# Performance work log

Measured on AMD Instinct MI355X. Metric: run time of the kernel, lower is better.

The kernel has to match this reference:

```python
import jax, jax.numpy as jnp
import numpy as np

INPUT_DIM = 512
EMBED_DIM = 64
B, S = 4, 4096


def setup_inputs() -> dict:
    key = jax.random.key(0)
    ks = jax.random.split(key, 9)
    scale = 1.0 / np.sqrt(INPUT_DIM)
    return {
        "q": jax.random.normal(ks[0], (B, S, INPUT_DIM), dtype=jnp.float32),
        "k": jax.random.normal(ks[1], (B, S, INPUT_DIM), dtype=jnp.float32),
        "v": jax.random.normal(ks[2], (B, S, INPUT_DIM), dtype=jnp.float32),
        "Wq": jax.random.uniform(ks[3], (INPUT_DIM, EMBED_DIM), jnp.float32, -scale, scale),
        "bq": jax.random.uniform(ks[4], (EMBED_DIM,), jnp.float32, -scale, scale),
        "Wk": jax.random.uniform(ks[5], (INPUT_DIM, EMBED_DIM), jnp.float32, -scale, scale),
        "bk": jax.random.uniform(ks[6], (EMBED_DIM,), jnp.float32, -scale, scale),
        "Wv": jax.random.uniform(ks[7], (INPUT_DIM, EMBED_DIM), jnp.float32, -scale, scale),
        "bv": jax.random.uniform(ks[8], (EMBED_DIM,), jnp.float32, -scale, scale),
    }


def reference(q, k, v, Wq, bq, Wk, bk, Wv, bv):
    # Linear projections (torch Linear: x @ W^T + b; here W stored as [in, out])
    Q = q @ Wq + bq  # [B, S, E]
    K = k @ Wk + bk  # [B, S, E]
    V = v @ Wv + bv  # [B, S, E]
    d_k = K.shape[-1]
    scores = jnp.einsum("bqe,bke->bqk", Q, K) / jnp.sqrt(jnp.float32(d_k))  # [B, S, S]
    attn = jax.nn.softmax(scores, axis=-1)
    return jnp.einsum("bqk,bke->bqe", attn, V)  # [B, S, E]
```

## Files before the change

### kernel.cpp

```cpp
#include <hip/hip_runtime.h>
#include <math.h>

#define S_ 4096
#define C_SCALE 0.18033688011112042f
#define KSPLIT 8

typedef __attribute__((ext_vector_type(4))) float  floatx4;
typedef __attribute__((ext_vector_type(4))) short  short4_t;
typedef __attribute__((ext_vector_type(8))) short  short8_t;
typedef __attribute__((ext_vector_type(4))) unsigned int uintx4;

__device__ __forceinline__ short f2bf(float f) {
  unsigned u = __builtin_bit_cast(unsigned, f);
  u += 0x7FFFu + ((u >> 16) & 1u);
  return (short)(u >> 16);
}
__device__ __forceinline__ unsigned pack2(float lo, float hi) {
  unsigned a = __builtin_bit_cast(unsigned, lo) + 0x8000u;
  unsigned b = __builtin_bit_cast(unsigned, hi) + 0x8000u;
  return __builtin_amdgcn_perm(b, a, 0x07060302u);
}
__device__ __forceinline__ unsigned packt(float lo, float hi) {
  return __builtin_amdgcn_perm(__builtin_bit_cast(unsigned, hi),
                               __builtin_bit_cast(unsigned, lo), 0x07060302u);
}
__device__ __forceinline__ float bf2f(short s) {
  return __builtin_bit_cast(float, (unsigned)((unsigned short)s) << 16);
}
__device__ __forceinline__ void dma16(const void* g, void* l) {
  __builtin_amdgcn_global_load_lds(
      (const __attribute__((address_space(1))) void*)g,
      (__attribute__((address_space(3))) void*)l, 16, 0, 0);
}

__global__ __launch_bounds__(256) void prep_w(const float* __restrict__ Wq,
                                              const float* __restrict__ Wk,
                                              const float* __restrict__ Wv,
                                              short* __restrict__ Wt) {
  __shared__ float T[64 * 65];
  int m = blockIdx.x >> 3, kt = blockIdx.x & 7, tid = threadIdx.x;
  const float* W = (m == 0) ? Wq : (m == 1) ? Wk : Wv;
  float sc = (m == 0) ? C_SCALE : 1.0f;
#pragma unroll
  for (int i = 0; i < 16; i++) {
    int e = i * 256 + tid;
    int k = e >> 6, n = e & 63;
    T[k * 65 + n] = W[(kt * 64 + k) * 64 + n];
  }
  __syncthreads();
#pragma unroll
  for (int i = 0; i < 16; i++) {
    int e = i * 256 + tid;
    int n = e >> 6, k = e & 63;
    Wt[m * 32768 + n * 512 + kt * 64 + k] = f2bf(T[k * 65 + n] * sc);
  }
}

__global__ __launch_bounds__(256, 3) void proj_kernel(
    const float* __restrict__ qin, const float* __restrict__ kin,
    const float* __restrict__ vin, const float* __restrict__ bq,
    const float* __restrict__ bk, const float* __restrict__ bv,
    const short* __restrict__ Wt, short* __restrict__ Qp,
    short* __restrict__ Kp, short* __restrict__ Vt) {
  __shared__ short A_lds[2][64 * 64];

  int tid = threadIdx.x;
  int m = blockIdx.x >> 8;
  int r0 = (blockIdx.x & 255) * 64;
  int wid = tid >> 6, lane = tid & 63, l15 = lane & 15, quad = lane >> 4;

  const float* in = (m == 0) ? qin : (m == 1) ? kin : vin;
  const short* Wm = Wt + m * 32768;

  short8_t wf[8][2];
#pragma unroll
  for (int kc = 0; kc < 8; kc++)
#pragma unroll
    for (int eh = 0; eh < 2; eh++)
      wf[kc][eh] = *(const short8_t*)(Wm + (wid * 16 + l15) * 512 + kc * 64 +
                                      eh * 32 + quad * 8);

  int sr = tid >> 3, sc = tid & 7;
  int sphys = (sc ^ (sr & 7)) * 8;

  floatx4 ar[4];
  auto loadA = [&](int kc) {
    const float* p = in + (size_t)(r0 + sr) * 512 + kc * 64 + sc * 8;
    ar[0] = *(const floatx4*)p;
    ar[1] = *(const floatx4*)(p + 4);
    const float* p2 = p + 32 * 512;
    ar[2] = *(const floatx4*)p2;
    ar[3] = *(const floatx4*)(p2 + 4);
  };

  floatx4 acc[4];
#pragma unroll
  for (int rt = 0; rt < 4; rt++) acc[rt] = (floatx4){0.f, 0.f, 0.f, 0.f};

  loadA(0);
#pragma unroll
  for (int kc = 0; kc < 8; kc++) {
    uintx4 w0 = {pack2(ar[0][0], ar[0][1]), pack2(ar[0][2], ar[0][3]),
                 pack2(ar[1][0], ar[1][1]), pack2(ar[1][2], ar[1][3])};
    uintx4 w1 = {pack2(ar[2][0], ar[2][1]), pack2(ar[2][2], ar[2][3]),
                 pack2(ar[3][0], ar[3][1]), pack2(ar[3][2], ar[3][3])};
    short* Ab = &A_lds[kc & 1][0];
    *(short8_t*)(Ab + sr * 64 + sphys) = __builtin_bit_cast(short8_t, w0);
    *(short8_t*)(Ab + (sr + 32) * 64 + sphys) = __builtin_bit_cast(short8_t, w1);
    __syncthreads();
    if (kc < 7) loadA(kc + 1);
    int akey = l15 & 7;
#pragma unroll
    for (int rt = 0; rt < 4; rt++) {
      int arow = rt * 16 + l15;
#pragma unroll
      for (int eh = 0; eh < 2; eh++) {
        short8_t af = *(const short8_t*)(Ab + arow * 64 + ((eh * 4 + quad) ^ akey) * 8);
        acc[rt] = __builtin_amdgcn_mfma_f32_16x16x32_bf16(af, wf[kc][eh], acc[rt], 0, 0, 0);
      }
    }
  }

  const float* bias = (m == 0) ? bq : (m == 1) ? bk : bv;
  float bsc = (m == 0) ? C_SCALE : 1.0f;
  float bv_ = bias[wid * 16 + l15] * bsc;
  if (m < 2) {
    short* out = (m == 0) ? Qp : Kp;
#pragma unroll
    for (int rt = 0; rt < 4; rt++)
#pragma unroll
      for (int r = 0; r < 4; r++)
        out[(size_t)(r0 + rt * 16 + quad * 4 + r) * 64 + wid * 16 + l15] =
            f2bf(acc[rt][r] + bv_);
  } else {
    int bb = r0 >> 12;
    int s0 = (r0 & 4095);
#pragma unroll
    for (int rt = 0; rt < 4; rt++) {
      short4_t pk = {f2bf(acc[rt][0] + bv_), f2bf(acc[rt][1] + bv_),
                     f2bf(acc[rt][2] + bv_), f2bf(acc[rt][3] + bv_)};
      *(short4_t*)(Vt + (size_t)bb * 262144 + (wid * 16 + l15) * 4096 + s0 +
                   rt * 16 + quad * 4) = pk;
    }
  }
}

__global__ __launch_bounds__(256, 2) void attn_kernel(
    const short* __restrict__ Qp, const short* __restrict__ Kp,
    const short* __restrict__ Vt, short* __restrict__ Po,
    float* __restrict__ Lp) {
  __shared__ short K_lds[2][64 * 64];
  __shared__ short V_lds[2][64 * 64];

  int tid = threadIdx.x;
  int ks = blockIdx.x >> 6, b = (blockIdx.x >> 4) & 3, qt = blockIdx.x & 15;
  int wid = tid >> 6, lane = tid & 63, l15 = lane & 15, quad = lane >> 4;

  const short* Qb = Qp + (size_t)b * (S_ * 64);
  const short* Kb = Kp + (size_t)b * (S_ * 64);
  const short* Vb = Vt + (size_t)b * (64 * S_);

  int q0 = qt * 256 + wid * 64;

  short8_t qf[4][2];
#pragma unroll
  for (int qs = 0; qs < 4; qs++)
#pragma unroll
    for (int h = 0; h < 2; h++)
      qf[qs][h] = *(const short8_t*)(Qb + (q0 + qs * 16 + l15) * 64 + h * 32 + quad * 8);

  floatx4 o[4][4];
#pragma unroll
  for (int qs = 0; qs < 4; qs++)
#pragma unroll
    for (int eb = 0; eb < 4; eb++) o[qs][eb] = (floatx4){0.f, 0.f, 0.f, 0.f};
  float l_acc[4] = {0.f, 0.f, 0.f, 0.f};
  int ks_base = ks * 512;

  auto stage = [&](int t, int buf) {
    int ks0 = ks_base + t * 64;
#pragma unroll
    for (int j = 0; j < 2; j++) {
      int slot = wid * 128 + j * 64 + lane;
      int r = slot >> 3, c = slot & 7;
      int kk = (r & 3) | (((r >> 3) & 1) << 2);
      dma16(Kb + (ks0 + r) * 64 + (c ^ kk) * 8, (void*)&K_lds[buf][(wid * 2 + j) * 512]);
      dma16(Vb + (size_t)r * 4096 + ks0 + (c ^ (r & 7)) * 8,
            (void*)&V_lds[buf][(wid * 2 + j) * 512]);
    }
  };

  stage(0, 0);
  for (int t = 0; t < 8; t++) {
    __syncthreads();
    if (t < 7) stage(t + 1, (t + 1) & 1);
    __syncthreads();
    const short* Kt = K_lds[t & 1];
    const short* Vl = V_lds[t & 1];

    int pr = 8 * (l15 >> 2) + (l15 & 3);
    int kkey = (l15 & 3) | (((l15 >> 2) & 1) << 2);

#pragma unroll
    for (int jg = 0; jg < 2; jg++) {
      const short* Kg = Kt + (jg * 32 + pr) * 64;
      short8_t kA0 = *(const short8_t*)(Kg + ((0 + quad) ^ kkey) * 8);
      short8_t kA1 = *(const short8_t*)(Kg + ((4 + quad) ^ kkey) * 8);
      short8_t kA2 = *(const short8_t*)(Kg + 256 + ((0 + quad) ^ kkey) * 8);
      short8_t kA3 = *(const short8_t*)(Kg + 256 + ((4 + quad) ^ kkey) * 8);
      short8_t vf[4];
#pragma unroll
      for (int eb = 0; eb < 4; eb++)
        vf[eb] = *(const short8_t*)(Vl + (eb * 16 + l15) * 64 +
                                    ((jg * 4 + quad) ^ (l15 & 7)) * 8);
#pragma unroll
      for (int qs = 0; qs < 4; qs++) {
        floatx4 z = (floatx4){0.f, 0.f, 0.f, 0.f};
        floatx4 s0 = __builtin_amdgcn_mfma_f32_16x16x32_bf16(kA0, qf[qs][0], z, 0, 0, 0);
        s0 = __builtin_amdgcn_mfma_f32_16x16x32_bf16(kA1, qf[qs][1], s0, 0, 0, 0);
        floatx4 s1 = __builtin_amdgcn_mfma_f32_16x16x32_bf16(kA2, qf[qs][0], z, 0, 0, 0);
        s1 = __builtin_amdgcn_mfma_f32_16x16x32_bf16(kA3, qf[qs][1], s1, 0, 0, 0);
        float e00 = __builtin_amdgcn_exp2f(s0[0]), e01 = __builtin_amdgcn_exp2f(s0[1]);
        float e02 = __builtin_amdgcn_exp2f(s0[2]), e03 = __builtin_amdgcn_exp2f(s0[3]);
        float e10 = __builtin_amdgcn_exp2f(s1[0]), e11 = __builtin_amdgcn_exp2f(s1[1]);
        float e12 = __builtin_amdgcn_exp2f(s1[2]), e13 = __builtin_amdgcn_exp2f(s1[3]);
        l_acc[qs] += ((e00 + e01) + (e02 + e03)) + ((e10 + e11) + (e12 + e13));
        uintx4 bp = {packt(e00, e01), packt(e02, e03),
                     packt(e10, e11), packt(e12, e13)};
        short8_t pB = __builtin_bit_cast(short8_t, bp);
#pragma unroll
        for (int eb = 0; eb < 4; eb++)
          o[qs][eb] = __builtin_amdgcn_mfma_f32_16x16x32_bf16(vf[eb], pB, o[qs][eb], 0, 0, 0);
      }
    }
  }

#pragma unroll
  for (int qs = 0; qs < 4; qs++) {
    float l = l_acc[qs];
    l += __shfl_xor(l, 16, 64);
    l += __shfl_xor(l, 32, 64);
    int grow = b * 4096 + q0 + qs * 16 + l15;
    short* Pb = Po + ((size_t)ks * 16384 + grow) * 64;
#pragma unroll
    for (int eb = 0; eb < 4; eb++) {
      short4_t pk = {f2bf(o[qs][eb][0]), f2bf(o[qs][eb][1]),
                     f2bf(o[qs][eb][2]), f2bf(o[qs][eb][3])};
      *(short4_t*)(Pb + eb * 16 + quad * 4) = pk;
    }
    if (quad == 0) Lp[ks * 16384 + grow] = l;
  }
}

__global__ __launch_bounds__(256) void combine_kernel(
    const short* __restrict__ Po, const float* __restrict__ Lp,
    float* __restrict__ out) {
  int gid = blockIdx.x * 256 + threadIdx.x;
  int grow = gid >> 3, e0 = (gid & 7) * 8;
  float s[8];
#pragma unroll
  for (int i = 0; i < 8; i++) s[i] = 0.f;
  float l = 0.f;
#pragma unroll
  for (int ks = 0; ks < KSPLIT; ks++) {
    short8_t p = *(const short8_t*)(Po + ((size_t)ks * 16384 + grow) * 64 + e0);
#pragma unroll
    for (int i = 0; i < 8; i++) s[i] += bf2f(p[i]);
    l += Lp[ks * 16384 + grow];
  }
  float inv = 1.0f / l;
  floatx4 o0 = {s[0] * inv, s[1] * inv, s[2] * inv, s[3] * inv};
  floatx4 o1 = {s[4] * inv, s[5] * inv, s[6] * inv, s[7] * inv};
  *(floatx4*)(out + (size_t)grow * 64 + e0) = o0;
  *(floatx4*)(out + (size_t)grow * 64 + e0 + 4) = o1;
}

extern "C" void kernel_launch(void* const* d_in, const int* in_sizes, int n_in,
                              void* d_out, int out_size, void* d_ws, size_t ws_size,
                              hipStream_t stream) {
  const float* q = (const float*)d_in[0];
  const float* k = (const float*)d_in[1];
  const float* v = (const float*)d_in[2];
  const float* Wq = (const float*)d_in[3];
  const float* bq = (const float*)d_in[4];
  const float* Wk = (const float*)d_in[5];
  const float* bk = (const float*)d_in[6];
  const float* Wv = (const float*)d_in[7];
  const float* bv = (const float*)d_in[8];

  char* ws = (char*)d_ws;
  short* Qp = (short*)(ws);
  short* Kp = (short*)(ws + (1u << 21));
  short* Vt = (short*)(ws + (2u << 21));
  short* Wt = (short*)(ws + (3u << 21));
  short* Po = (short*)(ws + (4u << 21));
  float* Lp = (float*)(ws + (13u << 21));

  prep_w<<<24, 256, 0, stream>>>(Wq, Wk, Wv, Wt);
  proj_kernel<<<768, 256, 0, stream>>>(q, k, v, bq, bk, bv, Wt, Qp, Kp, Vt);
  attn_kernel<<<512, 256, 0, stream>>>(Qp, Kp, Vt, Po, Lp);
  combine_kernel<<<512, 256, 0, stream>>>(Po, Lp, (float*)d_out);
}
```

Baseline: 168.3 us.

## Stage K/V through registers and compute softmax row sums with MFMA

```diff
diff --git a/kernel.cpp b/kernel.cpp
--- a/kernel.cpp
+++ b/kernel.cpp
@@ -26,11 +26,6 @@
 }
 __device__ __forceinline__ float bf2f(short s) {
   return __builtin_bit_cast(float, (unsigned)((unsigned short)s) << 16);
-}
-__device__ __forceinline__ void dma16(const void* g, void* l) {
-  __builtin_amdgcn_global_load_lds(
-      (const __attribute__((address_space(1))) void*)g,
-      (__attribute__((address_space(3))) void*)l, 16, 0, 0);
 }
 
 __global__ __launch_bounds__(256) void prep_w(const float* __restrict__ Wq,
@@ -170,36 +165,50 @@
       qf[qs][h] = *(const short8_t*)(Qb + (q0 + qs * 16 + l15) * 64 + h * 32 + quad * 8);
 
   floatx4 o[4][4];
-#pragma unroll
-  for (int qs = 0; qs < 4; qs++)
+  floatx4 ol[4];
+#pragma unroll
+  for (int qs = 0; qs < 4; qs++) {
+    ol[qs] = (floatx4){0.f, 0.f, 0.f, 0.f};
 #pragma unroll
     for (int eb = 0; eb < 4; eb++) o[qs][eb] = (floatx4){0.f, 0.f, 0.f, 0.f};
-  float l_acc[4] = {0.f, 0.f, 0.f, 0.f};
+  }
+
+  short8_t ones;
+#pragma unroll
+  for (int i = 0; i < 8; i++) ones[i] = (short)0x3F80;
+
+  int sr = tid >> 3, sc = tid & 7;
+  int kk = (sr & 3) | (((sr >> 3) & 1) << 2);
+  int vk = sr & 7;
+  short8_t kr0, kr1, vr0, vr1;
   int ks_base = ks * 512;
 
-  auto stage = [&](int t, int buf) {
+  auto loadKV = [&](int t) {
     int ks0 = ks_base + t * 64;
-#pragma unroll
-    for (int j = 0; j < 2; j++) {
-      int slot = wid * 128 + j * 64 + lane;
-      int r = slot >> 3, c = slot & 7;
-      int kk = (r & 3) | (((r >> 3) & 1) << 2);
-      dma16(Kb + (ks0 + r) * 64 + (c ^ kk) * 8, (void*)&K_lds[buf][(wid * 2 + j) * 512]);
-      dma16(Vb + (size_t)r * 4096 + ks0 + (c ^ (r & 7)) * 8,
-            (void*)&V_lds[buf][(wid * 2 + j) * 512]);
-    }
+    kr0 = *(const short8_t*)(Kb + (ks0 + sr) * 64 + sc * 8);
+    kr1 = *(const short8_t*)(Kb + (ks0 + sr + 32) * 64 + sc * 8);
+    vr0 = *(const short8_t*)(Vb + (size_t)sr * 4096 + ks0 + sc * 8);
+    vr1 = *(const short8_t*)(Vb + (size_t)(sr + 32) * 4096 + ks0 + sc * 8);
   };
-
-  stage(0, 0);
+  auto writeKV = [&](int buf) {
+    *(short8_t*)(&K_lds[buf][sr * 64 + ((sc ^ kk) * 8)]) = kr0;
+    *(short8_t*)(&K_lds[buf][(sr + 32) * 64 + ((sc ^ kk) * 8)]) = kr1;
+    *(short8_t*)(&V_lds[buf][sr * 64 + ((sc ^ vk) * 8)]) = vr0;
+    *(short8_t*)(&V_lds[buf][(sr + 32) * 64 + ((sc ^ vk) * 8)]) = vr1;
+  };
+
+  int pr = 8 * (l15 >> 2) + (l15 & 3);
+  int kkey = (l15 & 3) | (((l15 >> 2) & 1) << 2);
+  int vkey = l15 & 7;
+
+  loadKV(0);
+#pragma unroll
   for (int t = 0; t < 8; t++) {
+    writeKV(t & 1);
     __syncthreads();
-    if (t < 7) stage(t + 1, (t + 1) & 1);
-    __syncthreads();
-    const short* Kt = K_lds[t & 1];
-    const short* Vl = V_lds[t & 1];
-
-    int pr = 8 * (l15 >> 2) + (l15 & 3);
-    int kkey = (l15 & 3) | (((l15 >> 2) & 1) << 2);
+    if (t < 7) loadKV(t + 1);
+    const short* Kt = &K_lds[t & 1][0];
+    const short* Vl = &V_lds[t & 1][0];
 
 #pragma unroll
     for (int jg = 0; jg < 2; jg++) {
@@ -212,7 +221,7 @@
 #pragma unroll
       for (int eb = 0; eb < 4; eb++)
         vf[eb] = *(const short8_t*)(Vl + (eb * 16 + l15) * 64 +
-                                    ((jg * 4 + quad) ^ (l15 & 7)) * 8);
+                                    ((jg * 4 + quad) ^ vkey) * 8);
 #pragma unroll
       for (int qs = 0; qs < 4; qs++) {
         floatx4 z = (floatx4){0.f, 0.f, 0.f, 0.f};
@@ -224,22 +233,19 @@
         float e02 = __builtin_amdgcn_exp2f(s0[2]), e03 = __builtin_amdgcn_exp2f(s0[3]);
         float e10 = __builtin_amdgcn_exp2f(s1[0]), e11 = __builtin_amdgcn_exp2f(s1[1]);
         float e12 = __builtin_amdgcn_exp2f(s1[2]), e13 = __builtin_amdgcn_exp2f(s1[3]);
-        l_acc[qs] += ((e00 + e01) + (e02 + e03)) + ((e10 + e11) + (e12 + e13));
         uintx4 bp = {packt(e00, e01), packt(e02, e03),
                      packt(e10, e11), packt(e12, e13)};
         short8_t pB = __builtin_bit_cast(short8_t, bp);
 #pragma unroll
         for (int eb = 0; eb < 4; eb++)
           o[qs][eb] = __builtin_amdgcn_mfma_f32_16x16x32_bf16(vf[eb], pB, o[qs][eb], 0, 0, 0);
+        ol[qs] = __builtin_amdgcn_mfma_f32_16x16x32_bf16(ones, pB, ol[qs], 0, 0, 0);
       }
     }
   }
 
 #pragma unroll
   for (int qs = 0; qs < 4; qs++) {
-    float l = l_acc[qs];
-    l += __shfl_xor(l, 16, 64);
-    l += __shfl_xor(l, 32, 64);
     int grow = b * 4096 + q0 + qs * 16 + l15;
     short* Pb = Po + ((size_t)ks * 16384 + grow) * 64;
 #pragma unroll
@@ -248,7 +254,7 @@
                      f2bf(o[qs][eb][2]), f2bf(o[qs][eb][3])};
       *(short4_t*)(Pb + eb * 16 + quad * 4) = pk;
     }
-    if (quad == 0) Lp[ks * 16384 + grow] = l;
+    if (quad == 0) Lp[ks * 16384 + grow] = ol[qs][0];
   }
 }
 
```

Measured after the change: 168.3 us. Within noise of the previous version (-0.0%).
